# Kernel tuning notes

Measured on AMD Instinct MI355X. Metric: run time of the kernel, lower is better.

The kernel has to match this reference:

```python
import jax
import jax.numpy as jnp
from jax import lax
import numpy as np

VOCAB = 50000
EMB = 32
HID = 32
LAYERS = 4
BATCH = 8192
SEQ = 111


def setup_inputs() -> dict:
    key = jax.random.key(0)
    ks = jax.random.split(key, 12)
    s = 0.1
    x = jax.random.randint(ks[0], (BATCH, SEQ), 0, VOCAB, dtype=jnp.int64 if jax.config.read('jax_enable_x64') else jnp.int32)
    emb = jax.random.normal(ks[1], (VOCAB, EMB), jnp.float32) * s
    # stacked per-layer LSTM weights; layer-0 input dim == EMB == HID so stacking is valid
    Wih = jax.random.normal(ks[2], (LAYERS, 4 * HID, EMB), jnp.float32) * s
    Whh = jax.random.normal(ks[3], (LAYERS, 4 * HID, HID), jnp.float32) * s
    bih = jax.random.normal(ks[4], (LAYERS, 4 * HID), jnp.float32) * s
    bhh = jax.random.normal(ks[5], (LAYERS, 4 * HID), jnp.float32) * s
    Wa = jax.random.normal(ks[6], (HID, 1), jnp.float32) * s
    ba = jax.random.normal(ks[7], (1,), jnp.float32) * s
    W1 = jax.random.normal(ks[8], (HID, 32), jnp.float32) * s
    b1 = jax.random.normal(ks[9], (32,), jnp.float32) * s
    W2 = jax.random.normal(ks[10], (32, 3), jnp.float32) * s
    b2 = jax.random.normal(ks[11], (3,), jnp.float32) * s
    return {"x": x, "emb": emb, "Wih": Wih, "Whh": Whh, "bih": bih, "bhh": bhh,
            "Wa": Wa, "ba": ba, "W1": W1, "b1": b1, "W2": W2, "b2": b2}


def _lstm_layer(x, Wih, Whh, bih, bhh):
    # x: [B, T, D] -> [B, T, H]; PyTorch gate order: i, f, g, o
    B = x.shape[0]
    H = Whh.shape[1]
    # precompute the input contribution for all timesteps (one big GEMM)
    xg = jnp.einsum('btd,gd->btg', x, Wih) + bih + bhh  # [B, T, 4H]

    def step(carry, xg_t):
        h, c = carry
        z = xg_t + h @ Whh.T  # [B, 4H]
        i, f, g, o = jnp.split(z, 4, axis=-1)
        c = jax.nn.sigmoid(f) * c + jax.nn.sigmoid(i) * jnp.tanh(g)
        h = jax.nn.sigmoid(o) * jnp.tanh(c)
        return (h, c), h

    init = (jnp.zeros((B, H), x.dtype), jnp.zeros((B, H), x.dtype))
    _, hs = lax.scan(step, init, jnp.swapaxes(xg, 0, 1))  # hs: [T, B, H]
    return jnp.swapaxes(hs, 0, 1)


def reference(x, emb, Wih, Whh, bih, bhh, Wa, ba, W1, b1, W2, b2):
    h = emb[x]  # [B, T, E]
    for l in range(Wih.shape[0]):  # fixed 4 layers
        h = _lstm_layer(h, Wih[l], Whh[l], bih[l], bhh[l])
    scores = h @ Wa + ba                       # [B, T, 1]
    attn = jax.nn.softmax(scores, axis=1)      # softmax over time
    context = jnp.sum(h * attn, axis=1)        # [B, H]
    hid = jnp.tanh(context @ W1 + b1)          # dropout is identity at eval
    return hid @ W2 + b2                       # [B, 3]
```

## Files before the change

### kernel.cpp

```cpp
#include <hip/hip_runtime.h>

#define TSEQ 111
#define L2E 1.44269504088896340736f
#define TWO_L2E 2.88539008177792680472f

using f32x4  = __attribute__((ext_vector_type(4))) float;
using short8 = __attribute__((ext_vector_type(8))) short;

union FragU { unsigned u[4]; uint4 v; short8 s; };

__device__ __forceinline__ float fexp2(float x) { return __builtin_amdgcn_exp2f(x); }
__device__ __forceinline__ float frcp(float x)  { return __builtin_amdgcn_rcpf(x); }
__device__ __forceinline__ float tanh2(float zs) { return 1.f - 2.f * frcp(1.f + fexp2(zs + zs)); }

__device__ __forceinline__ unsigned rnd_bf16(float w) {
  unsigned u = __float_as_uint(w);
  return (u + 0x7fffu + ((u >> 16) & 1u)) >> 16;
}
__device__ __forceinline__ unsigned cvtpk(float a, float b) {
  unsigned r;
  asm("v_cvt_pk_bf16_f32 %0, %1, %2" : "=v"(r) : "v"(a), "v"(b));
  return r;
}

__global__ __launch_bounds__(512, 4) void lstm_fused(
    const int* __restrict__ x, const float* __restrict__ emb,
    const float* __restrict__ Wih, const float* __restrict__ Whh,
    const float* __restrict__ bih, const float* __restrict__ bhh,
    const float* __restrict__ Wa, const float* __restrict__ W1,
    const float* __restrict__ b1, const float* __restrict__ W2,
    const float* __restrict__ b2, float* __restrict__ out)
{
  __shared__ __align__(16) unsigned short hb[2 * 5 * 512];

  const int tid  = threadIdx.x;
  const int wvu  = __builtin_amdgcn_readfirstlane(tid) >> 6;
  const int l    = wvu >> 1;
  const int hf   = wvu & 1;
  const int lane = tid & 63;
  const int c    = lane & 15;
  const int q    = lane >> 4;
  const int gcc  = (c & 3) ^ (c >> 2);
  const int rowbase = blockIdx.x * 16;

  const int rdOff = c * 32 + ((q ^ gcc) << 3);
  const int u     = hf * 16 + c;
  const int uhi   = (u >> 3);
  const int ulo   = (u & 7);

  const int srow  = 2 * wvu + (lane >> 5);
  const int scol  = lane & 31;
  const int sgc   = (srow & 3) ^ (srow >> 2);
  const int sOff  = srow * 32 + ((((scol >> 3) ^ sgc)) << 3) + (scol & 7);
  const int sxrow = (rowbase + srow) * TSEQ;

  FragU wihf[4], whhf[4];
#pragma unroll
  for (int g = 0; g < 4; ++g) {
    const float sj = (g == 2) ? TWO_L2E : -L2E;
    const int j = 2 * g + hf;
    const float* srcI = Wih + l * 4096 + (16 * j + c) * 32 + 8 * q;
    const float* srcH = Whh + l * 4096 + (16 * j + c) * 32 + 8 * q;
#pragma unroll
    for (int p = 0; p < 4; ++p) {
      wihf[g].u[p] = rnd_bf16(srcI[2 * p] * sj) | (rnd_bf16(srcI[2 * p + 1] * sj) << 16);
      whhf[g].u[p] = rnd_bf16(srcH[2 * p] * sj) | (rnd_bf16(srcH[2 * p + 1] * sj) << 16);
    }
  }
  f32x4 bvv[4];
#pragma unroll
  for (int g = 0; g < 4; ++g) {
    const float sj = (g == 2) ? TWO_L2E : -L2E;
    const int j = 2 * g + hf;
    float b = (bih[l * 128 + 16 * j + c] + bhh[l * 128 + 16 * j + c]) * sj;
    bvv[g][0] = b; bvv[g][1] = b; bvv[g][2] = b; bvv[g][3] = b;
  }

  FragU wahA, walA;
#pragma unroll
  for (int p = 0; p < 4; ++p) { wahA.u[p] = 0u; walA.u[p] = 0u; }
  if (l == 1) {
#pragma unroll
    for (int p = 0; p < 4; ++p) {
      const int k0 = 8 * q + 2 * p;
      float w0 = Wa[k0] * L2E, w1 = Wa[k0 + 1] * L2E;
      unsigned h0 = rnd_bf16(w0), h1b = rnd_bf16(w1);
      wahA.u[p] = h0 | (h1b << 16);
      float l0 = w0 - __uint_as_float(h0 << 16);
      float l1 = w1 - __uint_as_float(h1b << 16);
      walA.u[p] = rnd_bf16(l0) | (rnd_bf16(l1) << 16);
    }
  }

  float cs[4];
#pragma unroll
  for (int e = 0; e < 4; ++e) cs[e] = 0.f;
  float mr = -1e30f, sr = 0.f, cx[4];
#pragma unroll
  for (int e = 0; e < 4; ++e) cx[e] = 0.f;

  for (int i = tid; i < 2 * 5 * 512 / 2; i += 512) ((unsigned*)hb)[i] = 0u;
  __syncthreads();

  {
    int i0 = x[sxrow];
    float e0 = emb[i0 * 32 + scol];
    hb[(1 * 5 + 0) * 512 + sOff] = (unsigned short)rnd_bf16(e0);
  }
  float embv = emb[x[sxrow + 1] * 32 + scol];
  int idxn = x[sxrow + 2];
  __syncthreads();

#pragma unroll 2
  for (int s = 0; s < TSEQ + 4; ++s) {
    const int t = s - l;
    const bool active = ((unsigned)t < (unsigned)TSEQ);
    const int rp = (s + 1) & 1;
    const int wp = s & 1;

    if (s + 1 < TSEQ) hb[(wp * 5 + 0) * 512 + sOff] = (unsigned short)rnd_bf16(embv);
    if (s + 2 < TSEQ) embv = emb[idxn * 32 + scol];
    if (s + 3 < TSEQ) idxn = x[sxrow + s + 3];

    FragU fi, fh, f3;
    if (active) {
      fi.v = *(const uint4*)(hb + (rp * 5 + l) * 512 + rdOff);
      fh.v = *(const uint4*)(hb + (rp * 5 + l + 1) * 512 + rdOff);
    }
    const bool doAtt = (l == 1) && (s >= 4);
    if (doAtt) f3.v = *(const uint4*)(hb + (rp * 5 + 4) * 512 + rdOff);

    if (active) {
      f32x4 acc[4];
#pragma unroll
      for (int g = 0; g < 4; ++g) {
        acc[g] = __builtin_amdgcn_mfma_f32_16x16x32_bf16(fi.s, wihf[g].s, bvv[g], 0, 0, 0);
        acc[g] = __builtin_amdgcn_mfma_f32_16x16x32_bf16(fh.s, whhf[g].s, acc[g], 0, 0, 0);
      }

      float hv[4];
#pragma unroll
      for (int e = 0; e < 4; ++e) {
        float a_ = fexp2(acc[0][e]);
        float m_ = fexp2(acc[1][e]);
        float b_ = fexp2(acc[2][e]);
        float p_ = fexp2(acc[3][e]);
        float P  = (1.f + a_) * (1.f + b_);
        float M1 = 1.f + m_;
        float cn = (cs[e] * P + (b_ - 1.f) * M1) * frcp(M1 * P);
        cs[e] = cn;
        float qv = fexp2(fminf(cn * TWO_L2E, 80.f));
        hv[e] = (qv - 1.f) * frcp((1.f + p_) * (1.f + qv));
      }

      {
        unsigned short* ob = hb + (wp * 5 + l + 1) * 512;
        unsigned u01 = cvtpk(hv[0], hv[1]);
        unsigned u23 = cvtpk(hv[2], hv[3]);
        const int r0 = 4 * q;
        ob[(r0 + 0) * 32 + (((uhi ^ (0 ^ q)) << 3) | ulo)] = (unsigned short)(u01 & 0xffffu);
        ob[(r0 + 1) * 32 + (((uhi ^ (1 ^ q)) << 3) | ulo)] = (unsigned short)(u01 >> 16);
        ob[(r0 + 2) * 32 + (((uhi ^ (2 ^ q)) << 3) | ulo)] = (unsigned short)(u23 & 0xffffu);
        ob[(r0 + 3) * 32 + (((uhi ^ (3 ^ q)) << 3) | ulo)] = (unsigned short)(u23 >> 16);
      }
    }

    if (doAtt) {
      f32x4 z = {0.f, 0.f, 0.f, 0.f};
      f32x4 sacc = __builtin_amdgcn_mfma_f32_16x16x32_bf16(wahA.s, f3.s, z, 0, 0, 0);
      sacc = __builtin_amdgcn_mfma_f32_16x16x32_bf16(walA.s, f3.s, sacc, 0, 0, 0);
      float pf = sacc[0];
      float mn = fmaxf(mr, pf);
      float sc = fexp2(mr - mn);
      float pr = fexp2(pf - mn);
      sr = sr * sc + pr;
#pragma unroll
      for (int p = 0; p < 2; ++p) {
        unsigned w = f3.u[2 * hf + p];
        float vlo = __uint_as_float(w << 16);
        float vhi = __uint_as_float(w & 0xffff0000u);
        cx[2 * p]     = cx[2 * p]     * sc + pr * vlo;
        cx[2 * p + 1] = cx[2 * p + 1] * sc + pr * vhi;
      }
      mr = mn;
    }

    asm volatile("s_waitcnt lgkmcnt(0)\n\ts_barrier" ::: "memory");
  }

  __syncthreads();

  float* cb = (float*)hb;
  if (l == 1) {
    float inv = frcp(sr);
#pragma unroll
    for (int e = 0; e < 4; ++e)
      cb[c * 33 + 8 * q + 4 * hf + e] = cx[e] * inv;
  }
  __syncthreads();
  if (wvu != 6) return;

  float a0[4], a1[4];
  {
    float bb0 = b1[c], bb1 = b1[c + 16];
#pragma unroll
    for (int e = 0; e < 4; ++e) { a0[e] = bb0; a1[e] = bb1; }
    for (int j = 0; j < 32; ++j) {
      float w0 = W1[j * 32 + c];
      float w1 = W1[j * 32 + c + 16];
#pragma unroll
      for (int e = 0; e < 4; ++e) {
        float cr = cb[(4 * q + e) * 33 + j];
        a0[e] = fmaf(cr, w0, a0[e]);
        a1[e] = fmaf(cr, w1, a1[e]);
      }
    }
  }
  float o0[4], o1[4], o2[4];
  {
    float w20 = W2[c * 3 + 0], w21 = W2[c * 3 + 1], w22 = W2[c * 3 + 2];
    float w30 = W2[(c + 16) * 3 + 0], w31 = W2[(c + 16) * 3 + 1], w32 = W2[(c + 16) * 3 + 2];
#pragma unroll
    for (int e = 0; e < 4; ++e) {
      float h0 = tanh2(a0[e] * L2E);
      float hB = tanh2(a1[e] * L2E);
      o0[e] = h0 * w20 + hB * w30;
      o1[e] = h0 * w21 + hB * w31;
      o2[e] = h0 * w22 + hB * w32;
    }
  }
#pragma unroll
  for (int mk = 1; mk <= 8; mk <<= 1) {
#pragma unroll
    for (int e = 0; e < 4; ++e) {
      o0[e] += __shfl_xor(o0[e], mk, 64);
      o1[e] += __shfl_xor(o1[e], mk, 64);
      o2[e] += __shfl_xor(o2[e], mk, 64);
    }
  }
  if (c < 3) {
    float bb = b2[c];
#pragma unroll
    for (int e = 0; e < 4; ++e) {
      float v = (c == 0) ? o0[e] : ((c == 1) ? o1[e] : o2[e]);
      out[(rowbase + 4 * q + e) * 3 + c] = v + bb;
    }
  }
}

extern "C" void kernel_launch(void* const* d_in, const int* in_sizes, int n_in,
                              void* d_out, int out_size, void* d_ws, size_t ws_size,
                              hipStream_t stream) {
  const int*   x   = (const int*)d_in[0];
  const float* emb = (const float*)d_in[1];
  const float* Wih = (const float*)d_in[2];
  const float* Whh = (const float*)d_in[3];
  const float* bih = (const float*)d_in[4];
  const float* bhh = (const float*)d_in[5];
  const float* Wa  = (const float*)d_in[6];
  const float* W1  = (const float*)d_in[8];
  const float* b1  = (const float*)d_in[9];
  const float* W2  = (const float*)d_in[10];
  const float* b2  = (const float*)d_in[11];
  float* out = (float*)d_out;

  lstm_fused<<<512, 512, 0, stream>>>(x, emb, Wih, Whh, bih, bhh, Wa, W1, b1, W2, b2, out);
}
```

Before: 167.5 us.

## Feed layer-0 embeddings directly from registers and move attention to layer-3 waves

Layer-0 waves now load embedding rows straight into registers as MFMA A-fragments instead of staging them through a shared-memory slot. That removes one LDS buffer per phase and the per-step store. Attention scoring moves to the layer-3 waves, which reuse their own recurrent h fragment instead of reading a separate slot. The cell math is recast into 2-wide vector ops, and s_setprio is raised around the MFMA section. The gathered embedding loads now sit on the recurrence critical path of layer 0, and the layer-3 waves take on the extra attention work.

```diff
diff --git a/kernel.cpp b/kernel.cpp
--- a/kernel.cpp
+++ b/kernel.cpp
@@ -5,6 +5,7 @@
 #define TWO_L2E 2.88539008177792680472f
 
 using f32x4  = __attribute__((ext_vector_type(4))) float;
+using f32x2  = __attribute__((ext_vector_type(2))) float;
 using short8 = __attribute__((ext_vector_type(8))) short;
 
 union FragU { unsigned u[4]; uint4 v; short8 s; };
@@ -12,6 +13,8 @@
 __device__ __forceinline__ float fexp2(float x) { return __builtin_amdgcn_exp2f(x); }
 __device__ __forceinline__ float frcp(float x)  { return __builtin_amdgcn_rcpf(x); }
 __device__ __forceinline__ float tanh2(float zs) { return 1.f - 2.f * frcp(1.f + fexp2(zs + zs)); }
+__device__ __forceinline__ f32x2 exp2v(f32x2 x) { f32x2 r; r[0] = fexp2(x[0]); r[1] = fexp2(x[1]); return r; }
+__device__ __forceinline__ f32x2 rcpv(f32x2 x)  { f32x2 r; r[0] = frcp(x[0]); r[1] = frcp(x[1]); return r; }
 
 __device__ __forceinline__ unsigned rnd_bf16(float w) {
   unsigned u = __float_as_uint(w);
@@ -31,7 +34,7 @@
     const float* __restrict__ b1, const float* __restrict__ W2,
     const float* __restrict__ b2, float* __restrict__ out)
 {
-  __shared__ __align__(16) unsigned short hb[2 * 5 * 512];
+  __shared__ __align__(16) unsigned short hb[2 * 4 * 512];
 
   const int tid  = threadIdx.x;
   const int wvu  = __builtin_amdgcn_readfirstlane(tid) >> 6;
@@ -42,17 +45,12 @@
   const int q    = lane >> 4;
   const int gcc  = (c & 3) ^ (c >> 2);
   const int rowbase = blockIdx.x * 16;
+  const int xrow = (rowbase + c) * TSEQ;
 
   const int rdOff = c * 32 + ((q ^ gcc) << 3);
   const int u     = hf * 16 + c;
   const int uhi   = (u >> 3);
   const int ulo   = (u & 7);
-
-  const int srow  = 2 * wvu + (lane >> 5);
-  const int scol  = lane & 31;
-  const int sgc   = (srow & 3) ^ (srow >> 2);
-  const int sOff  = srow * 32 + ((((scol >> 3) ^ sgc)) << 3) + (scol & 7);
-  const int sxrow = (rowbase + srow) * TSEQ;
 
   FragU wihf[4], whhf[4];
 #pragma unroll
@@ -79,36 +77,35 @@
   FragU wahA, walA;
 #pragma unroll
   for (int p = 0; p < 4; ++p) { wahA.u[p] = 0u; walA.u[p] = 0u; }
-  if (l == 1) {
+  if (l == 3) {
 #pragma unroll
     for (int p = 0; p < 4; ++p) {
       const int k0 = 8 * q + 2 * p;
       float w0 = Wa[k0] * L2E, w1 = Wa[k0 + 1] * L2E;
       unsigned h0 = rnd_bf16(w0), h1b = rnd_bf16(w1);
       wahA.u[p] = h0 | (h1b << 16);
-      float l0 = w0 - __uint_as_float(h0 << 16);
-      float l1 = w1 - __uint_as_float(h1b << 16);
-      walA.u[p] = rnd_bf16(l0) | (rnd_bf16(l1) << 16);
-    }
-  }
-
-  float cs[4];
-#pragma unroll
-  for (int e = 0; e < 4; ++e) cs[e] = 0.f;
+      float l0v = w0 - __uint_as_float(h0 << 16);
+      float l1v = w1 - __uint_as_float(h1b << 16);
+      walA.u[p] = rnd_bf16(l0v) | (rnd_bf16(l1v) << 16);
+    }
+  }
+
+  f32x2 cs2[2];
+  cs2[0] = (f32x2){0.f, 0.f}; cs2[1] = (f32x2){0.f, 0.f};
   float mr = -1e30f, sr = 0.f, cx[4];
 #pragma unroll
   for (int e = 0; e < 4; ++e) cx[e] = 0.f;
 
-  for (int i = tid; i < 2 * 5 * 512 / 2; i += 512) ((unsigned*)hb)[i] = 0u;
-  __syncthreads();
-
-  {
-    int i0 = x[sxrow];
-    float e0 = emb[i0 * 32 + scol];
-    hb[(1 * 5 + 0) * 512 + sOff] = (unsigned short)rnd_bf16(e0);
-  }
-  float embv = emb[x[sxrow + 1] * 32 + scol];
-  int idxn = x[sxrow + 2];
+  for (int i = tid; i < 2 * 4 * 512 / 2; i += 512) ((unsigned*)hb)[i] = 0u;
+
+  float4 emA = make_float4(0.f, 0.f, 0.f, 0.f), emB = emA;
+  int idxn = 0;
+  if (l == 0) {
+    int i0 = x[xrow];
+    emA = *(const float4*)(emb + i0 * 32 + 8 * q);
+    emB = *(const float4*)(emb + i0 * 32 + 8 * q + 4);
+    idxn = x[xrow + 1];
+  }
   __syncthreads();
 
 #pragma unroll 2
@@ -117,44 +114,68 @@
     const bool active = ((unsigned)t < (unsigned)TSEQ);
     const int rp = (s + 1) & 1;
     const int wp = s & 1;
-
-    if (s + 1 < TSEQ) hb[(wp * 5 + 0) * 512 + sOff] = (unsigned short)rnd_bf16(embv);
-    if (s + 2 < TSEQ) embv = emb[idxn * 32 + scol];
-    if (s + 3 < TSEQ) idxn = x[sxrow + s + 3];
-
-    FragU fi, fh, f3;
+    const bool doAtt = (l == 3) && (s >= 4);
+
+    FragU fi, fh;
+    __builtin_amdgcn_s_setprio(1);
     if (active) {
-      fi.v = *(const uint4*)(hb + (rp * 5 + l) * 512 + rdOff);
-      fh.v = *(const uint4*)(hb + (rp * 5 + l + 1) * 512 + rdOff);
-    }
-    const bool doAtt = (l == 1) && (s >= 4);
-    if (doAtt) f3.v = *(const uint4*)(hb + (rp * 5 + 4) * 512 + rdOff);
-
+      if (l == 0) {
+        fi.u[0] = cvtpk(emA.x, emA.y); fi.u[1] = cvtpk(emA.z, emA.w);
+        fi.u[2] = cvtpk(emB.x, emB.y); fi.u[3] = cvtpk(emB.z, emB.w);
+        if (t + 1 < TSEQ) {
+          emA = *(const float4*)(emb + idxn * 32 + 8 * q);
+          emB = *(const float4*)(emb + idxn * 32 + 8 * q + 4);
+        }
+        if (t + 2 < TSEQ) idxn = x[xrow + t + 2];
+      } else {
+        fi.v = *(const uint4*)(hb + (rp * 4 + (l - 1)) * 512 + rdOff);
+      }
+    }
+    if (active || doAtt)
+      fh.v = *(const uint4*)(hb + (rp * 4 + l) * 512 + rdOff);
+
+    f32x4 acc[4];
     if (active) {
-      f32x4 acc[4];
 #pragma unroll
       for (int g = 0; g < 4; ++g) {
         acc[g] = __builtin_amdgcn_mfma_f32_16x16x32_bf16(fi.s, wihf[g].s, bvv[g], 0, 0, 0);
         acc[g] = __builtin_amdgcn_mfma_f32_16x16x32_bf16(fh.s, whhf[g].s, acc[g], 0, 0, 0);
       }
-
+    }
+    f32x4 sacc;
+    if (doAtt) {
+      f32x4 z = {0.f, 0.f, 0.f, 0.f};
+      sacc = __builtin_amdgcn_mfma_f32_16x16x32_bf16(wahA.s, fh.s, z, 0, 0, 0);
+      sacc = __builtin_amdgcn_mfma_f32_16x16x32_bf16(walA.s, fh.s, sacc, 0, 0, 0);
+    }
+    __builtin_amdgcn_s_setprio(0);
+
+    if (active) {
       float hv[4];
-#pragma unroll
-      for (int e = 0; e < 4; ++e) {
-        float a_ = fexp2(acc[0][e]);
-        float m_ = fexp2(acc[1][e]);
-        float b_ = fexp2(acc[2][e]);
-        float p_ = fexp2(acc[3][e]);
-        float P  = (1.f + a_) * (1.f + b_);
-        float M1 = 1.f + m_;
-        float cn = (cs[e] * P + (b_ - 1.f) * M1) * frcp(M1 * P);
-        cs[e] = cn;
-        float qv = fexp2(fminf(cn * TWO_L2E, 80.f));
-        hv[e] = (qv - 1.f) * frcp((1.f + p_) * (1.f + qv));
+      const f32x2 one = {1.f, 1.f};
+      const f32x2 tl2 = {TWO_L2E, TWO_L2E};
+#pragma unroll
+      for (int pr2 = 0; pr2 < 2; ++pr2) {
+        const int e0 = 2 * pr2;
+        f32x2 va; va[0] = acc[0][e0]; va[1] = acc[0][e0 + 1];
+        f32x2 vm; vm[0] = acc[1][e0]; vm[1] = acc[1][e0 + 1];
+        f32x2 vb; vb[0] = acc[2][e0]; vb[1] = acc[2][e0 + 1];
+        f32x2 vp; vp[0] = acc[3][e0]; vp[1] = acc[3][e0 + 1];
+        f32x2 ea = exp2v(va), em_ = exp2v(vm), eb = exp2v(vb), ep = exp2v(vp);
+        f32x2 P  = (one + ea) * (one + eb);
+        f32x2 M1 = one + em_;
+        f32x2 num = cs2[pr2] * P + (eb - one) * M1;
+        f32x2 cn = num * rcpv(M1 * P);
+        cs2[pr2] = cn;
+        f32x2 qa = cn * tl2;
+        qa[0] = fminf(qa[0], 80.f); qa[1] = fminf(qa[1], 80.f);
+        f32x2 qv = exp2v(qa);
+        f32x2 hvv = (qv - one) * rcpv((one + ep) * (one + qv));
+        hv[e0] = hvv[0]; hv[e0 + 1] = hvv[1];
       }
 
       {
-        unsigned short* ob = hb + (wp * 5 + l + 1) * 512;
+        unsigned short* ob = hb + (wp * 4 + l) * 512;
         unsigned u01 = cvtpk(hv[0], hv[1]);
         unsigned u23 = cvtpk(hv[2], hv[3]);
         const int r0 = 4 * q;
@@ -166,9 +187,6 @@
     }
 
     if (doAtt) {
-      f32x4 z = {0.f, 0.f, 0.f, 0.f};
-      f32x4 sacc = __builtin_amdgcn_mfma_f32_16x16x32_bf16(wahA.s, f3.s, z, 0, 0, 0);
-      sacc = __builtin_amdgcn_mfma_f32_16x16x32_bf16(walA.s, f3.s, sacc, 0, 0, 0);
       float pf = sacc[0];
       float mn = fmaxf(mr, pf);
       float sc = fexp2(mr - mn);
@@ -176,7 +194,7 @@
       sr = sr * sc + pr;
 #pragma unroll
       for (int p = 0; p < 2; ++p) {
-        unsigned w = f3.u[2 * hf + p];
+        unsigned w = fh.u[2 * hf + p];
         float vlo = __uint_as_float(w << 16);
         float vhi = __uint_as_float(w & 0xffff0000u);
         cx[2 * p]     = cx[2 * p]     * sc + pr * vlo;
@@ -191,7 +209,7 @@
   __syncthreads();
 
   float* cb = (float*)hb;
-  if (l == 1) {
+  if (l == 3) {
     float inv = frcp(sr);
 #pragma unroll
     for (int e = 0; e < 4; ++e)
```

Result: no change. 165.4 us (-1.2%).
